# Optimization experiments

Measured on AMD Instinct MI355X. Metric: run time of the kernel, lower is better.

Reference implementation:

```python
import jax, jax.numpy as jnp
import numpy as np

Q_STAGES = 8      # residual VQ stages
K_CODES = 1024    # codebook size per stage
D = 256           # code dim == encoder channels


def setup_inputs() -> dict:
    key = jax.random.key(0)
    ks = jax.random.split(key, 6)
    B, T = 8, 8192
    x = jax.random.normal(ks[0], (B, 1, T), dtype=jnp.float32)
    enc_w = jax.random.normal(ks[1], (D, 1, 3), dtype=jnp.float32) * 0.3
    enc_b = jnp.zeros((D,), dtype=jnp.float32)
    dec_w = jax.random.normal(ks[2], (1, D, 3), dtype=jnp.float32) * (1.0 / np.sqrt(3 * D))
    dec_b = jnp.zeros((1,), dtype=jnp.float32)
    codebooks = jax.random.normal(ks[3], (Q_STAGES, K_CODES, D), dtype=jnp.float32)
    return {"x": x, "enc_w": enc_w, "enc_b": enc_b,
            "dec_w": dec_w, "dec_b": dec_b, "codebooks": codebooks}


def _conv1d(x, w, b):
    # x: [B,C,T], w: [O,I,3], 'same' padding
    y = jax.lax.conv_general_dilated(x, w, window_strides=(1,), padding='SAME',
                                     dimension_numbers=('NCH', 'OIH', 'NCH'))
    return y + b[None, :, None]


def _rvq(z, codebooks):
    # z: [B,D,T] -> tokens [N,D]
    B, d, T = z.shape
    flat = jnp.transpose(z, (0, 2, 1)).reshape(B * T, d)  # [N,D]

    def stage(carry, cb):
        residual, quant_sum, loss = carry
        r2 = jnp.sum(residual * residual, axis=1, keepdims=True)      # [N,1]
        c2 = jnp.sum(cb * cb, axis=1)                                  # [K]
        dist = r2 - 2.0 * (residual @ cb.T) + c2[None, :]              # [N,K]
        idx = jnp.argmin(dist, axis=1)                                 # [N]
        q = jax.lax.stop_gradient(cb[idx])                             # [N,D]
        loss = loss + jnp.mean((residual - q) ** 2)                    # commitment
        return (residual - q, quant_sum + q, loss), None

    init = (flat, jnp.zeros_like(flat), jnp.float32(0.0))
    (res, quant_sum, loss), _ = jax.lax.scan(stage, init, codebooks)
    # straight-through estimator
    quant = flat + jax.lax.stop_gradient(quant_sum - flat)
    quant = jnp.transpose(quant.reshape(B, T, d), (0, 2, 1))           # [B,D,T]
    return quant, loss


def reference(x, enc_w, enc_b, dec_w, dec_b, codebooks):
    encoded = _conv1d(x, enc_w, enc_b)              # [B,256,T]
    quantized, commit_loss = _rvq(encoded, codebooks)
    decoded = _conv1d(quantized, dec_w, dec_b)      # [B,1,T]
    return decoded, commit_loss
```

## Files before the change

### kernel.cpp

```cpp
#include <hip/hip_runtime.h>

#define QS 8
#define KC 1024
#define DD 256
#define TT 8192
#define NN 65536
#define TAU 0.06f

typedef _Float16 half8 __attribute__((ext_vector_type(8)));
typedef float f32x4 __attribute__((ext_vector_type(4)));

__device__ __forceinline__ void gload_lds16(const _Float16* g, _Float16* l) {
    __builtin_amdgcn_global_load_lds(
        (const __attribute__((address_space(1))) void*)g,
        (__attribute__((address_space(3))) void*)l,
        16, 0, 0);
}

__global__ __launch_bounds__(256) void cb_prep_all_kernel(
    const float* __restrict__ cbs, _Float16* __restrict__ cbh)
{
    const int b = blockIdx.x, s = b >> 6, t = b & 63;
    const int cg = t >> 2, kp = t & 3;
    const float* cb = cbs + (size_t)s * KC * DD;
    _Float16* dst = cbh + (size_t)s * KC * DD + (size_t)t * 4096;
    #pragma unroll
    for (int q = 0; q < 2; ++q) {
        const int p = threadIdx.x + 256*q;
        const int code = p & 63, kchunk = p >> 6;
        const float* src = &cb[(long)(cg*64 + code)*DD + kp*64 + kchunk*8];
        const float4 v0 = *reinterpret_cast<const float4*>(src);
        const float4 v1 = *reinterpret_cast<const float4*>(src + 4);
        half8 hv;
        hv[0]=(_Float16)v0.x; hv[1]=(_Float16)v0.y;
        hv[2]=(_Float16)v0.z; hv[3]=(_Float16)v0.w;
        hv[4]=(_Float16)v1.x; hv[5]=(_Float16)v1.y;
        hv[6]=(_Float16)v1.z; hv[7]=(_Float16)v1.w;
        *reinterpret_cast<half8*>(&dst[p*8]) = hv;
    }
}

__global__ __launch_bounds__(256) void c2_kernel(
    const float* __restrict__ cbs, float* __restrict__ c2,
    float* __restrict__ lossAcc)
{
    if (blockIdx.x == 0 && threadIdx.x == 0) *lossAcc = 0.0f;
    const int w = (int)((blockIdx.x * blockDim.x + threadIdx.x) >> 6);
    const int lane = threadIdx.x & 63;
    if (w >= QS * KC) return;
    const float* row = cbs + (long)w * DD;
    float s = 0.0f;
    #pragma unroll
    for (int q = 0; q < DD / 64; ++q) {
        const float v = row[lane + 64*q];
        s += v * v;
    }
    #pragma unroll
    for (int off = 32; off; off >>= 1) s += __shfl_down(s, off, 64);
    if (lane == 0) c2[w] = s;
}

__global__ __launch_bounds__(512, 2) void mega_kernel(
    const float* __restrict__ x,   const float* __restrict__ ew,
    const float* __restrict__ eb,  const float* __restrict__ cbs,
    const _Float16* __restrict__ cbh, const float* __restrict__ c2,
    _Float16* __restrict__ resf,   float* __restrict__ lossAcc)
{
    __shared__ __align__(16) _Float16 Bt[4][4096];
    __shared__ int   idxArr[128];
    __shared__ float rrow[DD];
    __shared__ float sD8[8];
    __shared__ int   sI8[8];
    __shared__ int   flagRows[64];
    __shared__ int   flagCnt;

    const int tid = threadIdx.x;
    const int w   = tid >> 6;
    const int l   = tid & 63;
    const int l15 = l & 15;
    const int l4  = l >> 4;
    const int n0  = blockIdx.x * 128;
    const int n   = n0 + w*16 + l15;

    int tr;
    {
        half8 pa, pb;
        #pragma unroll
        for (int e = 0; e < 8; ++e) {
            pa[e] = (_Float16)l15;
            pb[e] = (_Float16)0.03125f;
        }
        f32x4 pacc = (f32x4){0.f, 0.f, 0.f, 0.f};
        pacc = __builtin_amdgcn_mfma_f32_16x16x32_f16(pa, pb, pacc, 0, 0, 0);
        const float p1 = __shfl(pacc[1], 0, 64);
        tr = (p1 < 0.5f) ? 1 : 0;
    }

    float r[8][8];
    {
        const int t = n & (TT - 1);
        const float xm = (t > 0)      ? x[n - 1] : 0.0f;
        const float x0v = x[n];
        const float xp = (t < TT - 1) ? x[n + 1] : 0.0f;
        #pragma unroll
        for (int kc = 0; kc < 8; ++kc)
            #pragma unroll
            for (int e = 0; e < 8; ++e) {
                const int d = kc*32 + l4*8 + e;
                r[kc][e] = eb[d] + ew[3*d]*xm + ew[3*d+1]*x0v + ew[3*d+2]*xp;
            }
    }

    float lsum = 0.0f;
    half8 ah[8], al[8];

    for (int s = 0; s < QS; ++s) {
        const _Float16* cbhS = cbh + (size_t)s * KC * DD;
        const float*    cbS  = cbs + (size_t)s * KC * DD;
        const float*    c2S  = c2 + s * KC;

        #pragma unroll
        for (int kc = 0; kc < 8; ++kc) {
            half8 hv, lv;
            #pragma unroll
            for (int e = 0; e < 8; ++e) {
                const _Float16 hh = (_Float16)r[kc][e];
                hv[e] = hh;
                lv[e] = (_Float16)(r[kc][e] - (float)hh);
            }
            ah[kc] = hv; al[kc] = lv;
        }

        if (tid == 0) flagCnt = 0;

        float b1[4], b2[4]; int i1[4];
        #pragma unroll
        for (int q = 0; q < 4; ++q) { b1[q] = 1e30f; b2[q] = 1e30f; i1[q] = 0; }

        gload_lds16(cbhS + 0*4096 + tid*8, &Bt[0][w*512]);
        gload_lds16(cbhS + 1*4096 + tid*8, &Bt[1][w*512]);
        gload_lds16(cbhS + 2*4096 + tid*8, &Bt[2][w*512]);

        for (int cg = 0; cg < 16; ++cg) {
            f32x4 acc[4];
            #pragma unroll
            for (int nt = 0; nt < 4; ++nt) acc[nt] = (f32x4){0.f,0.f,0.f,0.f};

            for (int kp = 0; kp < 4; ++kp) {
                const int t = cg*4 + kp, buf = t & 3;
                if (t < 62)      asm volatile("s_waitcnt vmcnt(2)" ::: "memory");
                else if (t==62)  asm volatile("s_waitcnt vmcnt(1)" ::: "memory");
                else             asm volatile("s_waitcnt vmcnt(0)" ::: "memory");
                __builtin_amdgcn_sched_barrier(0);
                __builtin_amdgcn_s_barrier();
                __builtin_amdgcn_sched_barrier(0);

                if (t < 61)
                    gload_lds16(cbhS + (size_t)(t+3)*4096 + tid*8, &Bt[(t+3)&3][w*512]);

                #pragma unroll
                for (int kc2 = 0; kc2 < 2; ++kc2) {
                    const int kc = kp*2 + kc2;
                    #pragma unroll
                    for (int nt = 0; nt < 4; ++nt) {
                        const int slot = ((kc2*4 + l4)*64 + nt*16 + l15)*8;
                        const half8 bh = *reinterpret_cast<const half8*>(&Bt[buf][slot]);
                        acc[nt] = __builtin_amdgcn_mfma_f32_16x16x32_f16(ah[kc], bh, acc[nt], 0, 0, 0);
                        acc[nt] = __builtin_amdgcn_mfma_f32_16x16x32_f16(al[kc], bh, acc[nt], 0, 0, 0);
                    }
                }
            }

            if (tr == 0) {
                #pragma unroll
                for (int nt = 0; nt < 4; ++nt) {
                    const int code = cg*64 + nt*16 + l15;
                    const float cc = c2S[code];
                    #pragma unroll
                    for (int j = 0; j < 4; ++j) {
                        const float dist = cc - 2.0f*acc[nt][j];
                        if (dist < b1[j])      { b2[j] = b1[j]; b1[j] = dist; i1[j] = code; }
                        else if (dist < b2[j]) { b2[j] = dist; }
                    }
                }
            } else {
                #pragma unroll
                for (int nt = 0; nt < 4; ++nt) {
                    #pragma unroll
                    for (int j = 0; j < 4; ++j) {
                        const int code = cg*64 + nt*16 + l4*4 + j;
                        const float dist = c2S[code] - 2.0f*acc[nt][j];
                        if (dist < b1[0])      { b2[0] = b1[0]; b1[0] = dist; i1[0] = code; }
                        else if (dist < b2[0]) { b2[0] = dist; }
                    }
                }
            }
        }

        if (tr == 0) {
            #pragma unroll
            for (int m = 1; m < 16; m <<= 1) {
                #pragma unroll
                for (int q = 0; q < 4; ++q) {
                    const float ob1 = __shfl_xor(b1[q], m, 64);
                    const float ob2 = __shfl_xor(b2[q], m, 64);
                    const int   oi1 = __shfl_xor(i1[q], m, 64);
                    const float nb2 = fminf(fminf(b2[q], ob2), fmaxf(b1[q], ob1));
                    if (ob1 < b1[q] || (ob1 == b1[q] && oi1 < i1[q])) { b1[q] = ob1; i1[q] = oi1; }
                    b2[q] = nb2;
                }
            }
            if (l15 == 0) {
                #pragma unroll
                for (int j = 0; j < 4; ++j) {
                    const int row = w*16 + l4*4 + j;
                    idxArr[row] = i1[j];
                    if (b2[j] - b1[j] < TAU) {
                        const int pos = atomicAdd(&flagCnt, 1);
                        if (pos < 64) flagRows[pos] = row;
                    }
                }
            }
        } else {
            #pragma unroll
            for (int m = 16; m <= 32; m <<= 1) {
                const float ob1 = __shfl_xor(b1[0], m, 64);
                const float ob2 = __shfl_xor(b2[0], m, 64);
                const int   oi1 = __shfl_xor(i1[0], m, 64);
                const float nb2 = fminf(fminf(b2[0], ob2), fmaxf(b1[0], ob1));
                if (ob1 < b1[0] || (ob1 == b1[0] && oi1 < i1[0])) { b1[0] = ob1; i1[0] = oi1; }
                b2[0] = nb2;
            }
            if (l4 == 0) {
                const int row = w*16 + l15;
                idxArr[row] = i1[0];
                if (b2[0] - b1[0] < TAU) {
                    const int pos = atomicAdd(&flagCnt, 1);
                    if (pos < 64) flagRows[pos] = row;
                }
            }
        }
        __syncthreads();

        const int fc = min(flagCnt, 64);
        for (int f = 0; f < fc; ++f) {
            const int row = flagRows[f];
            if (w == (row >> 4) && l15 == (row & 15)) {
                #pragma unroll
                for (int kc = 0; kc < 8; ++kc)
                    #pragma unroll
                    for (int e = 0; e < 8; ++e)
                        rrow[kc*32 + l4*8 + e] = r[kc][e];
            }
            __syncthreads();
            float bd = 1e30f; int bi = 0;
            #pragma unroll
            for (int q = 0; q < 2; ++q) {
                const int code = tid*2 + q;
                const float* crow = cbS + (size_t)code * DD;
                float dot = 0.f;
                for (int d4 = 0; d4 < DD; d4 += 4) {
                    const float4 cv = *reinterpret_cast<const float4*>(&crow[d4]);
                    dot += rrow[d4]*cv.x + rrow[d4+1]*cv.y
                         + rrow[d4+2]*cv.z + rrow[d4+3]*cv.w;
                }
                const float dist = c2S[code] - 2.0f*dot;
                if (dist < bd || (dist == bd && code < bi)) { bd = dist; bi = code; }
            }
            #pragma unroll
            for (int off = 32; off; off >>= 1) {
                const float od = __shfl_down(bd, off, 64);
                const int   oi = __shfl_down(bi, off, 64);
                if (od < bd || (od == bd && oi < bi)) { bd = od; bi = oi; }
            }
            if (l == 0) { sD8[w] = bd; sI8[w] = bi; }
            __syncthreads();
            if (tid == 0) {
                float fbd = sD8[0]; int fbi = sI8[0];
                #pragma unroll
                for (int ww = 1; ww < 8; ++ww) {
                    if (sD8[ww] < fbd || (sD8[ww] == fbd && sI8[ww] < fbi)) {
                        fbd = sD8[ww]; fbi = sI8[ww];
                    }
                }
                idxArr[row] = fbi;
            }
            __syncthreads();
        }

        const int ix = idxArr[w*16 + l15];
        const float* crow = cbS + (size_t)ix * DD;
        #pragma unroll
        for (int kc = 0; kc < 8; ++kc) {
            const float4 c0 = *reinterpret_cast<const float4*>(&crow[kc*32 + l4*8]);
            const float4 c1 = *reinterpret_cast<const float4*>(&crow[kc*32 + l4*8 + 4]);
            r[kc][0] -= c0.x; r[kc][1] -= c0.y; r[kc][2] -= c0.z; r[kc][3] -= c0.w;
            r[kc][4] -= c1.x; r[kc][5] -= c1.y; r[kc][6] -= c1.z; r[kc][7] -= c1.w;
            #pragma unroll
            for (int e = 0; e < 8; ++e) lsum += r[kc][e]*r[kc][e];
        }
    }

    #pragma unroll
    for (int kc = 0; kc < 8; ++kc) {
        half8 hv;
        #pragma unroll
        for (int e = 0; e < 8; ++e) hv[e] = (_Float16)r[kc][e];
        *reinterpret_cast<half8*>(&resf[(size_t)n*DD + kc*32 + l4*8]) = hv;
    }
    #pragma unroll
    for (int off = 32; off; off >>= 1) lsum += __shfl_down(lsum, off, 64);
    if (l == 0) atomicAdd(lossAcc, lsum);
}

__global__ __launch_bounds__(256) void decode_kernel(
    const float* __restrict__ x,  const float* __restrict__ ew,
    const float* __restrict__ eb, const _Float16* __restrict__ resf,
    const float* __restrict__ dw, const float* __restrict__ db,
    const float* __restrict__ lossAcc, float* __restrict__ out)
{
    const long n = (long)blockIdx.x * 4 + (threadIdx.x >> 6);
    const int lane = threadIdx.x & 63;
    const int t = (int)(n & (TT - 1));
    float sum = 0.0f;
    #pragma unroll
    for (int k = 0; k < 3; ++k) {
        const int tm = t + k - 1;
        if (tm < 0 || tm > TT - 1) continue;
        const long m = n + k - 1;
        const float xm = (tm > 0)      ? x[m - 1] : 0.0f;
        const float x0 = x[m];
        const float xp = (tm < TT - 1) ? x[m + 1] : 0.0f;
        #pragma unroll
        for (int q = 0; q < 4; ++q) {
            const int d = lane + 64 * q;
            const float z = eb[d] + ew[d*3]*xm + ew[d*3 + 1]*x0 + ew[d*3 + 2]*xp;
            const float quant = z - (float)resf[m * DD + d];
            sum += quant * dw[d*3 + k];
        }
    }
    #pragma unroll
    for (int off = 32; off; off >>= 1) sum += __shfl_down(sum, off, 64);
    if (lane == 0) out[n] = sum + db[0];
    if (blockIdx.x == 0 && threadIdx.x == 0)
        out[NN] = lossAcc[0] * (1.0f / ((float)NN * (float)DD));
}

extern "C" void kernel_launch(void* const* d_in, const int* in_sizes, int n_in,
                              void* d_out, int out_size, void* d_ws, size_t ws_size,
                              hipStream_t stream)
{
    const float* x     = (const float*)d_in[0];
    const float* enc_w = (const float*)d_in[1];
    const float* enc_b = (const float*)d_in[2];
    const float* dec_w = (const float*)d_in[3];
    const float* dec_b = (const float*)d_in[4];
    const float* cbs   = (const float*)d_in[5];
    float* out = (float*)d_out;

    _Float16* resf    = (_Float16*)d_ws;
    _Float16* cbh     = resf + (size_t)NN * DD;
    float*    lossAcc = (float*)(cbh + (size_t)QS * KC * DD);
    float*    c2      = out + 8;

    hipLaunchKernelGGL(cb_prep_all_kernel, dim3(QS * 64), dim3(256), 0, stream,
                       cbs, cbh);
    hipLaunchKernelGGL(c2_kernel, dim3(QS * KC / 4), dim3(256), 0, stream,
                       cbs, c2, lossAcc);
    hipLaunchKernelGGL(mega_kernel, dim3(NN / 128), dim3(512), 0, stream,
                       x, enc_w, enc_b, cbs, cbh, c2, resf, lossAcc);
    hipLaunchKernelGGL(decode_kernel, dim3(NN / 4), dim3(256), 0, stream,
                       x, enc_w, enc_b, resf, dec_w, dec_b, lossAcc, out);
}
```

Baseline: 1.534 ms.

## Drop LDS codebook staging, load pre-swizzled fp16 codebook straight to registers

```diff
diff --git a/kernel.cpp b/kernel.cpp
--- a/kernel.cpp
+++ b/kernel.cpp
@@ -10,13 +10,6 @@
 typedef _Float16 half8 __attribute__((ext_vector_type(8)));
 typedef float f32x4 __attribute__((ext_vector_type(4)));
 
-__device__ __forceinline__ void gload_lds16(const _Float16* g, _Float16* l) {
-    __builtin_amdgcn_global_load_lds(
-        (const __attribute__((address_space(1))) void*)g,
-        (__attribute__((address_space(3))) void*)l,
-        16, 0, 0);
-}
-
 __global__ __launch_bounds__(256) void cb_prep_all_kernel(
     const float* __restrict__ cbs, _Float16* __restrict__ cbh)
 {
@@ -27,8 +20,11 @@
     #pragma unroll
     for (int q = 0; q < 2; ++q) {
         const int p = threadIdx.x + 256*q;
-        const int code = p & 63, kchunk = p >> 6;
-        const float* src = &cb[(long)(cg*64 + code)*DD + kp*64 + kchunk*8];
+        const int kc2 = p >> 8, rem = p & 255;
+        const int nt = rem >> 6, l4v = (rem >> 4) & 3, l15v = rem & 15;
+        const int code = cg*64 + nt*16 + l15v;
+        const int k0 = kp*64 + kc2*32 + l4v*8;
+        const float* src = &cb[(long)code*DD + k0];
         const float4 v0 = *reinterpret_cast<const float4*>(src);
         const float4 v1 = *reinterpret_cast<const float4*>(src + 4);
         half8 hv;
@@ -36,7 +32,8 @@
         hv[2]=(_Float16)v0.z; hv[3]=(_Float16)v0.w;
         hv[4]=(_Float16)v1.x; hv[5]=(_Float16)v1.y;
         hv[6]=(_Float16)v1.z; hv[7]=(_Float16)v1.w;
-        *reinterpret_cast<half8*>(&dst[p*8]) = hv;
+        *reinterpret_cast<half8*>(
+            &dst[(kc2*4 + nt)*512 + (l4v*16 + l15v)*8]) = hv;
     }
 }
 
@@ -60,18 +57,17 @@
     if (lane == 0) c2[w] = s;
 }
 
-__global__ __launch_bounds__(512, 2) void mega_kernel(
+__global__ __launch_bounds__(512, 4) void mega_kernel(
     const float* __restrict__ x,   const float* __restrict__ ew,
     const float* __restrict__ eb,  const float* __restrict__ cbs,
-    const _Float16* __restrict__ cbh, const float* __restrict__ c2,
+    const _Float16* __restrict__ cbh, const float* __restrict__ c2all,
     _Float16* __restrict__ resf,   float* __restrict__ lossAcc)
 {
-    __shared__ __align__(16) _Float16 Bt[4][4096];
     __shared__ int   idxArr[128];
     __shared__ float rrow[DD];
     __shared__ float sD8[8];
     __shared__ int   sI8[8];
-    __shared__ int   flagRows[64];
+    __shared__ int   flagRows[128];
     __shared__ int   flagCnt;
 
     const int tid = threadIdx.x;
@@ -96,77 +92,55 @@
         tr = (p1 < 0.5f) ? 1 : 0;
     }
 
-    float r[8][8];
+    half8 ah[8], al[8];
     {
         const int t = n & (TT - 1);
         const float xm = (t > 0)      ? x[n - 1] : 0.0f;
         const float x0v = x[n];
         const float xp = (t < TT - 1) ? x[n + 1] : 0.0f;
         #pragma unroll
-        for (int kc = 0; kc < 8; ++kc)
+        for (int kc = 0; kc < 8; ++kc) {
             #pragma unroll
             for (int e = 0; e < 8; ++e) {
                 const int d = kc*32 + l4*8 + e;
-                r[kc][e] = eb[d] + ew[3*d]*xm + ew[3*d+1]*x0v + ew[3*d+2]*xp;
-            }
+                const float z = eb[d] + ew[3*d]*xm + ew[3*d+1]*x0v + ew[3*d+2]*xp;
+                const _Float16 hh = (_Float16)z;
+                ah[kc][e] = hh;
+                al[kc][e] = (_Float16)(z - (float)hh);
+            }
+        }
     }
 
     float lsum = 0.0f;
-    half8 ah[8], al[8];
 
     for (int s = 0; s < QS; ++s) {
-        const _Float16* cbhS = cbh + (size_t)s * KC * DD;
+        const _Float16* cbhL = cbh + (size_t)s * KC * DD + l*8;
         const float*    cbS  = cbs + (size_t)s * KC * DD;
-        const float*    c2S  = c2 + s * KC;
-
-        #pragma unroll
-        for (int kc = 0; kc < 8; ++kc) {
-            half8 hv, lv;
-            #pragma unroll
-            for (int e = 0; e < 8; ++e) {
-                const _Float16 hh = (_Float16)r[kc][e];
-                hv[e] = hh;
-                lv[e] = (_Float16)(r[kc][e] - (float)hh);
-            }
-            ah[kc] = hv; al[kc] = lv;
-        }
-
-        if (tid == 0) flagCnt = 0;
+        const float*    c2S  = c2all + s * KC;
 
         float b1[4], b2[4]; int i1[4];
         #pragma unroll
-        for (int q = 0; q < 4; ++q) { b1[q] = 1e30f; b2[q] = 1e30f; i1[q] = 0; }
-
-        gload_lds16(cbhS + 0*4096 + tid*8, &Bt[0][w*512]);
-        gload_lds16(cbhS + 1*4096 + tid*8, &Bt[1][w*512]);
-        gload_lds16(cbhS + 2*4096 + tid*8, &Bt[2][w*512]);
+        for (int r = 0; r < 4; ++r) { b1[r] = 1e30f; b2[r] = 1e30f; i1[r] = 0; }
+
+        f32x4 acc[4];
+        half8 bA[4];
 
         for (int cg = 0; cg < 16; ++cg) {
-            f32x4 acc[4];
             #pragma unroll
             for (int nt = 0; nt < 4; ++nt) acc[nt] = (f32x4){0.f,0.f,0.f,0.f};
 
             for (int kp = 0; kp < 4; ++kp) {
-                const int t = cg*4 + kp, buf = t & 3;
-                if (t < 62)      asm volatile("s_waitcnt vmcnt(2)" ::: "memory");
-                else if (t==62)  asm volatile("s_waitcnt vmcnt(1)" ::: "memory");
-                else             asm volatile("s_waitcnt vmcnt(0)" ::: "memory");
-                __builtin_amdgcn_sched_barrier(0);
-                __builtin_amdgcn_s_barrier();
-                __builtin_amdgcn_sched_barrier(0);
-
-                if (t < 61)
-                    gload_lds16(cbhS + (size_t)(t+3)*4096 + tid*8, &Bt[(t+3)&3][w*512]);
-
+                const _Float16* base = cbhL + (long)(cg*4 + kp)*4096;
                 #pragma unroll
                 for (int kc2 = 0; kc2 < 2; ++kc2) {
                     const int kc = kp*2 + kc2;
                     #pragma unroll
+                    for (int f = 0; f < 4; ++f)
+                        bA[f] = *reinterpret_cast<const half8*>(base + (kc2*4 + f)*512);
+                    #pragma unroll
                     for (int nt = 0; nt < 4; ++nt) {
-                        const int slot = ((kc2*4 + l4)*64 + nt*16 + l15)*8;
-                        const half8 bh = *reinterpret_cast<const half8*>(&Bt[buf][slot]);
-                        acc[nt] = __builtin_amdgcn_mfma_f32_16x16x32_f16(ah[kc], bh, acc[nt], 0, 0, 0);
-                        acc[nt] = __builtin_amdgcn_mfma_f32_16x16x32_f16(al[kc], bh, acc[nt], 0, 0, 0);
+                        acc[nt] = __builtin_amdgcn_mfma_f32_16x16x32_f16(ah[kc], bA[nt], acc[nt], 0, 0, 0);
+                        acc[nt] = __builtin_amdgcn_mfma_f32_16x16x32_f16(al[kc], bA[nt], acc[nt], 0, 0, 0);
                     }
                 }
             }
@@ -178,9 +152,11 @@
                     const float cc = c2S[code];
                     #pragma unroll
                     for (int j = 0; j < 4; ++j) {
-                        const float dist = cc - 2.0f*acc[nt][j];
-                        if (dist < b1[j])      { b2[j] = b1[j]; b1[j] = dist; i1[j] = code; }
-                        else if (dist < b2[j]) { b2[j] = dist; }
+                        const float dist = fmaf(-2.0f, acc[nt][j], cc);
+                        const bool lt = dist < b1[j];
+                        b2[j] = fminf(b2[j], fmaxf(b1[j], dist));
+                        b1[j] = lt ? dist : b1[j];
+                        i1[j] = lt ? code : i1[j];
                     }
                 }
             } else {
@@ -189,25 +165,31 @@
                     #pragma unroll
                     for (int j = 0; j < 4; ++j) {
                         const int code = cg*64 + nt*16 + l4*4 + j;
-                        const float dist = c2S[code] - 2.0f*acc[nt][j];
-                        if (dist < b1[0])      { b2[0] = b1[0]; b1[0] = dist; i1[0] = code; }
-                        else if (dist < b2[0]) { b2[0] = dist; }
-                    }
-                }
-            }
-        }
+                        const float dist = fmaf(-2.0f, acc[nt][j], c2S[code]);
+                        const bool lt = dist < b1[0];
+                        b2[0] = fminf(b2[0], fmaxf(b1[0], dist));
+                        b1[0] = lt ? dist : b1[0];
+                        i1[0] = lt ? code : i1[0];
+                    }
+                }
+            }
+        }
+
+        __syncthreads();
+        if (tid == 0) flagCnt = 0;
+        __syncthreads();
 
         if (tr == 0) {
             #pragma unroll
             for (int m = 1; m < 16; m <<= 1) {
                 #pragma unroll
-                for (int q = 0; q < 4; ++q) {
-                    const float ob1 = __shfl_xor(b1[q], m, 64);
-                    const float ob2 = __shfl_xor(b2[q], m, 64);
-                    const int   oi1 = __shfl_xor(i1[q], m, 64);
-                    const float nb2 = fminf(fminf(b2[q], ob2), fmaxf(b1[q], ob1));
-                    if (ob1 < b1[q] || (ob1 == b1[q] && oi1 < i1[q])) { b1[q] = ob1; i1[q] = oi1; }
-                    b2[q] = nb2;
+                for (int r = 0; r < 4; ++r) {
+                    const float ob1 = __shfl_xor(b1[r], m, 64);
+                    const float ob2 = __shfl_xor(b2[r], m, 64);
+                    const int   oi1 = __shfl_xor(i1[r], m, 64);
+                    const float nb2 = fminf(fminf(b2[r], ob2), fmaxf(b1[r], ob1));
+                    if (ob1 < b1[r] || (ob1 == b1[r] && oi1 < i1[r])) { b1[r] = ob1; i1[r] = oi1; }
+                    b2[r] = nb2;
                 }
             }
             if (l15 == 0) {
@@ -217,7 +199,7 @@
                     idxArr[row] = i1[j];
                     if (b2[j] - b1[j] < TAU) {
                         const int pos = atomicAdd(&flagCnt, 1);
-                        if (pos < 64) flagRows[pos] = row;
+                        flagRows[pos] = row;
                     }
                 }
             }
@@ -236,13 +218,13 @@
                 idxArr[row] = i1[0];
                 if (b2[0] - b1[0] < TAU) {
                     const int pos = atomicAdd(&flagCnt, 1);
-                    if (pos < 64) flagRows[pos] = row;
+                    flagRows[pos] = row;
                 }
             }
         }
         __syncthreads();
 
-        const int fc = min(flagCnt, 64);
+        const int fc = flagCnt;
         for (int f = 0; f < fc; ++f) {
             const int row = flagRows[f];
             if (w == (row >> 4) && l15 == (row & 15)) {
@@ -250,7 +232,7 @@
                 for (int kc = 0; kc < 8; ++kc)
                     #pragma unroll
                     for (int e = 0; e < 8; ++e)
-                        rrow[kc*32 + l4*8 + e] = r[kc][e];
+                        rrow[kc*32 + l4*8 + e] = (float)ah[kc][e] + (float)al[kc][e];
             }
             __syncthreads();
             float bd = 1e30f; int bi = 0;
@@ -294,10 +276,15 @@
         for (int kc = 0; kc < 8; ++kc) {
             const float4 c0 = *reinterpret_cast<const float4*>(&crow[kc*32 + l4*8]);
             const float4 c1 = *reinterpret_cast<const float4*>(&crow[kc*32 + l4*8 + 4]);
-            r[kc][0] -= c0.x; r[kc][1] -= c0.y; r[kc][2] -= c0.z; r[kc][3] -= c0.w;
-            r[kc][4] -= c1.x; r[kc][5] -= c1.y; r[kc][6] -= c1.z; r[kc][7] -= c1.w;
-            #pragma unroll
-            for (int e = 0; e < 8; ++e) lsum += r[kc][e]*r[kc][e];
+            const float cv[8] = {c0.x, c0.y, c0.z, c0.w, c1.x, c1.y, c1.z, c1.w};
+            #pragma unroll
+            for (int e = 0; e < 8; ++e) {
+                const float rv = ((float)ah[kc][e] + (float)al[kc][e]) - cv[e];
+                lsum += rv * rv;
+                const _Float16 hh = (_Float16)rv;
+                ah[kc][e] = hh;
+                al[kc][e] = (_Float16)(rv - (float)hh);
+            }
         }
     }
 
@@ -305,7 +292,8 @@
     for (int kc = 0; kc < 8; ++kc) {
         half8 hv;
         #pragma unroll
-        for (int e = 0; e < 8; ++e) hv[e] = (_Float16)r[kc][e];
+        for (int e = 0; e < 8; ++e)
+            hv[e] = (_Float16)((float)ah[kc][e] + (float)al[kc][e]);
         *reinterpret_cast<half8*>(&resf[(size_t)n*DD + kc*32 + l4*8]) = hv;
     }
     #pragma unroll
```

Measured after the change: 1.457 ms. -5.0%, faster.
